# Optimization experiments

Measured on AMD Instinct MI355X. Metric: run time of the kernel, lower is better.

## Reference

```python
import jax, jax.numpy as jnp
import numpy as np

N, D = 2048, 1024
H, KV, HD = 16, 4, 64
REPEATS = H // KV
SCALE = HD ** -0.5


def setup_inputs() -> dict:
    key = jax.random.key(0)
    ks = jax.random.split(key, 6)
    x = jax.random.normal(ks[0], (N, D), dtype=jnp.float32)
    # rotary tables: cos/sin of interleaved-pair angles (llama-style view_as_complex)
    pos = jnp.arange(N, dtype=jnp.float32)[:, None]
    inv_freq = 1.0 / (10000.0 ** (jnp.arange(0, HD, 2, dtype=jnp.float32) / HD))
    ang = pos * inv_freq[None, :]  # (N, HD//2)
    freqs_cos = jnp.cos(ang)
    freqs_sin = jnp.sin(ang)
    s = 0.02
    Wq = jax.random.normal(ks[1], (D, H * HD), dtype=jnp.float32) * s
    Wk = jax.random.normal(ks[2], (D, KV * HD), dtype=jnp.float32) * s
    Wv = jax.random.normal(ks[3], (D, KV * HD), dtype=jnp.float32) * s
    Wo = jax.random.normal(ks[4], (H * HD, D), dtype=jnp.float32) * s
    return {"x": x, "freqs_cos": freqs_cos, "freqs_sin": freqs_sin,
            "Wq": Wq, "Wk": Wk, "Wv": Wv, "Wo": Wo}


def _rope(t, cos, sin):
    # t: (N, heads, HD); interleaved complex pairs (even=real, odd=imag)
    tr = t[..., 0::2]
    ti = t[..., 1::2]
    c = cos[:, None, :]
    s = sin[:, None, :]
    out_r = tr * c - ti * s
    out_i = tr * s + ti * c
    return jnp.stack([out_r, out_i], axis=-1).reshape(t.shape)


def reference(x, freqs_cos, freqs_sin, Wq, Wk, Wv, Wo):
    n = x.shape[0]
    xq = (x @ Wq).reshape(n, H, HD)
    xk = (x @ Wk).reshape(n, KV, HD)
    xv = (x @ Wv).reshape(n, KV, HD)
    xq = _rope(xq, freqs_cos, freqs_sin)
    xk = _rope(xk, freqs_cos, freqs_sin)
    # repeat_kv along head dim (GQA)
    k = jnp.repeat(xk, REPEATS, axis=1)  # (n, H, HD)
    v = jnp.repeat(xv, REPEATS, axis=1)
    # memory_efficient_attention with mask=None: full attention over token axis
    scores = jnp.einsum('nhd,mhd->hnm', xq, k) * SCALE
    attn = jax.nn.softmax(scores, axis=-1)
    out = jnp.einsum('hnm,mhd->nhd', attn, v)
    return out.reshape(n, H * HD) @ Wo
```

## Files before the change

### kernel.cpp

```cpp
#include <hip/hip_runtime.h>

#define N_TOK 2048
#define DMODEL 1024
#define NH 16
#define NKV 4
#define HDIM 64
#define SCALE_LOG2E 0.1803368801111204f

typedef __attribute__((ext_vector_type(8))) short short8;
typedef __attribute__((ext_vector_type(4))) float f32x4;
typedef __attribute__((ext_vector_type(16))) float f32x16;
typedef unsigned short u16;
typedef unsigned int u32;

__device__ __forceinline__ u16 f2bf(float x) {
    u32 u = __float_as_uint(x);
    u += 0x7FFF + ((u >> 16) & 1);
    return (u16)(u >> 16);
}
__device__ __forceinline__ u32 pack2(float a, float b) {
    return (u32)f2bf(a) | ((u32)f2bf(b) << 16);
}
__device__ __forceinline__ u32 pack2t(float a, float b) {
    return __builtin_amdgcn_perm(__float_as_uint(b), __float_as_uint(a), 0x07060302u);
}

__device__ __forceinline__ void gload16(const u16* g, u16* l) {
    __builtin_amdgcn_global_load_lds(
        (const __attribute__((address_space(1))) unsigned int*)g,
        (__attribute__((address_space(3))) unsigned int*)l, 16, 0, 0);
}

__global__ __launch_bounds__(256) void prep(
    const float* __restrict__ Wq, const float* __restrict__ Wk,
    const float* __restrict__ Wv, const float* __restrict__ Wo,
    const float* __restrict__ x,
    u16* __restrict__ Wqt, u16* __restrict__ Wkt, u16* __restrict__ Wvt,
    u16* __restrict__ Wot, u16* __restrict__ xb)
{
    const int z = blockIdx.z;
    const int t = threadIdx.x;
    if (z == 4) {
        size_t base = ((size_t)(blockIdx.y * 16 + blockIdx.x)) * 8192;
#pragma unroll
        for (int i = 0; i < 8; ++i) {
            float4 v = *(const float4*)(x + base + i * 1024 + t * 4);
            uint2 p; p.x = pack2(v.x, v.y); p.y = pack2(v.z, v.w);
            *(uint2*)(xb + base + i * 1024 + t * 4) = p;
        }
        return;
    }
    const float* W; u16* Wt; int NC;
    if      (z == 0) { W = Wq; Wt = Wqt; NC = 1024; }
    else if (z == 1) { W = Wk; Wt = Wkt; NC = 256; }
    else if (z == 2) { W = Wv; Wt = Wvt; NC = 256; }
    else             { W = Wo; Wt = Wot; NC = 1024; }
    const int n0 = blockIdx.x * 64;
    if (n0 >= NC) return;
    const int k0 = blockIdx.y * 64;
    __shared__ float T[64][68];
    const int row = t >> 2, cs = (t & 3) * 16;
#pragma unroll
    for (int i = 0; i < 4; ++i)
        *(float4*)&T[row][cs + i * 4] =
            *(const float4*)(W + (size_t)(k0 + row) * NC + n0 + cs + i * 4);
    __syncthreads();
    const int nl = t >> 2, ks = (t & 3) * 16;
    u32 pk[8];
#pragma unroll
    for (int i = 0; i < 8; ++i)
        pk[i] = pack2(T[ks + 2 * i][nl], T[ks + 2 * i + 1][nl]);
    u16* dst = Wt + (size_t)(n0 + nl) * DMODEL + k0 + ks;
    uint4 w0; w0.x = pk[0]; w0.y = pk[1]; w0.z = pk[2]; w0.w = pk[3];
    uint4 w1; w1.x = pk[4]; w1.y = pk[5]; w1.z = pk[6]; w1.w = pk[7];
    *(uint4*)(dst) = w0;
    *(uint4*)(dst + 8) = w1;
}

__global__ __launch_bounds__(256, 3) void gemm_qkv(
    const u16* __restrict__ A,
    const u16* __restrict__ B0, const u16* __restrict__ B1, const u16* __restrict__ B2,
    u16* __restrict__ D0, u16* __restrict__ D1, u16* __restrict__ FVout,
    const float* __restrict__ fc, const float* __restrict__ fs)
{
    __shared__ u16 As[2][64][64];
    __shared__ u16 Bs[2][64][64];
    const int t = threadIdx.x;
    const int m0 = blockIdx.x * 64;
    const int by = blockIdx.y;

    const u16* Bt; int nl0, ep;
    u16* dbf = nullptr; int dstride = 0; float epsc = 1.f;
    if (by < 16)      { Bt = B0; nl0 = by * 64;        dbf = D0; ep = 1; dstride = 1024;
                        epsc = SCALE_LOG2E; }
    else if (by < 20) { Bt = B1; nl0 = (by - 16) * 64; dbf = D1; ep = 1; dstride = 256; }
    else              { Bt = B2; nl0 = (by - 20) * 64; ep = 2; }

    const int w = t >> 6, lane = t & 63;
    const int quad = lane >> 4, l15 = lane & 15;
    const int wm = (w >> 1) * 32, wn = (w & 1) * 32;
    const int rx = l15 & 7;

    const int sro = w * 16 + (lane >> 3);
    const int sco = ((lane & 7) ^ (lane >> 3)) * 8;
    const u16* ApL = A + (size_t)(m0 + sro) * DMODEL + sco;
    const u16* BpL = Bt + (size_t)(nl0 + sro) * DMODEL + sco;

    f32x4 acc[2][2];
#pragma unroll
    for (int i = 0; i < 2; ++i)
#pragma unroll
        for (int j = 0; j < 2; ++j) acc[i][j] = {0.f, 0.f, 0.f, 0.f};

#pragma unroll
    for (int k = 0; k < 2; ++k) {
        gload16(ApL + k * 8 * DMODEL, &As[0][w * 16 + k * 8][0]);
        gload16(BpL + k * 8 * DMODEL, &Bs[0][w * 16 + k * 8][0]);
    }
    __syncthreads();

    for (int it = 0; it < 16; ++it) {
        const int cur = it & 1;
        if (it + 1 < 16) {
            const int kk = (it + 1) * 64;
#pragma unroll
            for (int k = 0; k < 2; ++k) {
                gload16(ApL + k * 8 * DMODEL + kk, &As[cur ^ 1][w * 16 + k * 8][0]);
                gload16(BpL + k * 8 * DMODEL + kk, &Bs[cur ^ 1][w * 16 + k * 8][0]);
            }
        }
#pragma unroll
        for (int c = 0; c < 2; ++c) {
            short8 af[2], bf[2];
#pragma unroll
            for (int i = 0; i < 2; ++i)
                af[i] = *(const short8*)&As[cur][wm + i * 16 + l15][((4 * c + quad) ^ rx) * 8];
#pragma unroll
            for (int j = 0; j < 2; ++j)
                bf[j] = *(const short8*)&Bs[cur][wn + j * 16 + l15][((4 * c + quad) ^ rx) * 8];
#pragma unroll
            for (int i = 0; i < 2; ++i)
#pragma unroll
                for (int j = 0; j < 2; ++j)
                    acc[i][j] = __builtin_amdgcn_mfma_f32_16x16x32_bf16(af[i], bf[j], acc[i][j], 0, 0, 0);
        }
        __syncthreads();
    }

#pragma unroll
    for (int i = 0; i < 2; ++i)
#pragma unroll
        for (int j = 0; j < 2; ++j) {
            const int cl = nl0 + wn + j * 16 + l15;
            if (ep == 1) {
#pragma unroll
                for (int r4 = 0; r4 < 4; ++r4) {
                    const int r = m0 + wm + i * 16 + quad * 4 + r4;
                    float own = acc[i][j][r4];
                    float other = __shfl_xor(own, 1, 64);
                    const int p = (cl & 63) >> 1;
                    const float c = fc[r * 32 + p] * epsc, s = fs[r * 32 + p] * epsc;
                    float outv = ((cl & 1) == 0) ? (own * c - other * s)
                                                 : (other * s + own * c);
                    dbf[(size_t)r * dstride + cl] = f2bf(outv);
                }
            } else {
                const int rb = m0 + wm + i * 16 + quad * 4;
                const int g = cl >> 6, d = cl & 63;
                const int d2 = d >> 5, dl = d & 31;
                const int keyblk = rb >> 7, kg = (rb >> 5) & 3;
                const int kst = (rb >> 4) & 1, hb = (rb >> 3) & 1, jv = rb & 7;
                size_t idx = ((((((size_t)(g * 16 + keyblk) * 4 + kg) * 2 + kst) * 2 + d2)
                               * 2 + hb) * 32 + dl) * 8 + jv;
                uint2 pk;
                pk.x = pack2(acc[i][j][0], acc[i][j][1]);
                pk.y = pack2(acc[i][j][2], acc[i][j][3]);
                *(uint2*)(FVout + idx) = pk;
            }
        }
}

__global__ __launch_bounds__(256, 2) void gemm_out(
    const u16* __restrict__ A, const u16* __restrict__ Bt, float* __restrict__ Dout)
{
    __shared__ u16 As[2][64][64];
    __shared__ u16 Bs[2][64][64];
    const int t = threadIdx.x;
    const int m0 = blockIdx.x * 64;
    const int nl0 = blockIdx.y * 64;

    const int w = t >> 6, lane = t & 63;
    const int quad = lane >> 4, l15 = lane & 15;
    const int wm = (w >> 1) * 32, wn = (w & 1) * 32;
    const int rx = l15 & 7;

    const int sro = w * 16 + (lane >> 3);
    const int sco = ((lane & 7) ^ (lane >> 3)) * 8;
    const u16* ApL = A + (size_t)(m0 + sro) * DMODEL + sco;
    const u16* BpL = Bt + (size_t)(nl0 + sro) * DMODEL + sco;

    f32x4 acc[2][2];
#pragma unroll
    for (int i = 0; i < 2; ++i)
#pragma unroll
        for (int j = 0; j < 2; ++j) acc[i][j] = {0.f, 0.f, 0.f, 0.f};

#pragma unroll
    for (int k = 0; k < 2; ++k) {
        gload16(ApL + k * 8 * DMODEL, &As[0][w * 16 + k * 8][0]);
        gload16(BpL + k * 8 * DMODEL, &Bs[0][w * 16 + k * 8][0]);
    }
    __syncthreads();

    for (int it = 0; it < 16; ++it) {
        const int cur = it & 1;
        if (it + 1 < 16) {
            const int kk = (it + 1) * 64;
#pragma unroll
            for (int k = 0; k < 2; ++k) {
                gload16(ApL + k * 8 * DMODEL + kk, &As[cur ^ 1][w * 16 + k * 8][0]);
                gload16(BpL + k * 8 * DMODEL + kk, &Bs[cur ^ 1][w * 16 + k * 8][0]);
            }
        }
#pragma unroll
        for (int c = 0; c < 2; ++c) {
            short8 af[2], bf[2];
#pragma unroll
            for (int i = 0; i < 2; ++i)
                af[i] = *(const short8*)&As[cur][wm + i * 16 + l15][((4 * c + quad) ^ rx) * 8];
#pragma unroll
            for (int j = 0; j < 2; ++j)
                bf[j] = *(const short8*)&Bs[cur][wn + j * 16 + l15][((4 * c + quad) ^ rx) * 8];
#pragma unroll
            for (int i = 0; i < 2; ++i)
#pragma unroll
                for (int j = 0; j < 2; ++j)
                    acc[i][j] = __builtin_amdgcn_mfma_f32_16x16x32_bf16(af[i], bf[j], acc[i][j], 0, 0, 0);
        }
        __syncthreads();
    }

#pragma unroll
    for (int i = 0; i < 2; ++i)
#pragma unroll
        for (int j = 0; j < 2; ++j) {
            const int cl = nl0 + wn + j * 16 + l15;
#pragma unroll
            for (int r4 = 0; r4 < 4; ++r4) {
                const int r = m0 + wm + i * 16 + quad * 4 + r4;
                Dout[(size_t)r * 1024 + cl] = acc[i][j][r4];
            }
        }
}

__global__ __launch_bounds__(256, 2) void attn(
    const u16* __restrict__ Qb, const u16* __restrict__ Kb,
    const u16* __restrict__ FV, u16* __restrict__ Ob)
{
    __shared__ u16 Ks[2][2][64][72];
    __shared__ u16 Ps[4][32][40];

    const int t = threadIdx.x;
    const int n0 = blockIdx.x * 64;
    const int h = blockIdx.y, kvh = h >> 2;
    const int w = t >> 6, lane = t & 63;
    const int hi = lane >> 5, l31 = lane & 31;
    const int qgrp = w & 1, khalf = w >> 1;
    const int srow = t >> 1, ssel = (t & 1) * 32;
    const int khalf_s = srow >> 6, klocal = srow & 63;

    const short8 ones = {(short)0x3F80, (short)0x3F80, (short)0x3F80, (short)0x3F80,
                         (short)0x3F80, (short)0x3F80, (short)0x3F80, (short)0x3F80};

    const u16* qp = Qb + (size_t)(n0 + qgrp * 32 + l31) * (NH * HDIM) + h * HDIM + hi * 8;
    short8 qf[4];
#pragma unroll
    for (int s = 0; s < 4; ++s) qf[s] = *(const short8*)(qp + s * 16);

    const u16* kbase = Kb + (size_t)(khalf_s * 1024 + klocal) * (NKV * HDIM) + kvh * HDIM + ssel;
    const u16* fvb = FV + ((size_t)kvh * 16 * 8192) + (size_t)lane * 8;

    f32x16 o[2], o_l;
#pragma unroll
    for (int d2 = 0; d2 < 2; ++d2)
#pragma unroll
        for (int r = 0; r < 16; ++r) o[d2][r] = 0.f;
#pragma unroll
    for (int r = 0; r < 16; ++r) o_l[r] = 0.f;

#pragma unroll
    for (int c = 0; c < 4; ++c)
        *(uint4*)&Ks[0][khalf_s][klocal][ssel + c * 8] = *(const uint4*)(kbase + c * 8);
    __syncthreads();

    for (int rd = 0; rd < 16; ++rd) {
        const int cur = rd & 1, nxt = cur ^ 1;
        const int rdn = (rd + 1) & 15;
        uint4 kr[4];
#pragma unroll
        for (int c = 0; c < 4; ++c)
            kr[c] = *(const uint4*)(kbase + (size_t)(rdn * 64) * (NKV * HDIM) + c * 8);

#pragma unroll
        for (int kg = 0; kg < 2; ++kg) {
            const int kg_global = khalf * 32 + rd * 2 + kg;
            const int keyblk = kg_global >> 2, kgi = kg_global & 3;
            short8 vf[2][2];
#pragma unroll
            for (int s = 0; s < 2; ++s)
#pragma unroll
                for (int d2 = 0; d2 < 2; ++d2)
                    vf[s][d2] = *(const short8*)(fvb +
                        ((((size_t)keyblk * 4 + kgi) * 2 + s) * 2 + d2) * 512);
            f32x16 sa;
#pragma unroll
            for (int r = 0; r < 16; ++r) sa[r] = 0.f;
#pragma unroll
            for (int s = 0; s < 4; ++s) {
                short8 kf = *(const short8*)&Ks[cur][khalf][kg * 32 + l31][s * 16 + hi * 8];
                sa = __builtin_amdgcn_mfma_f32_32x32x16_bf16(kf, qf[s], sa, 0, 0, 0);
            }
            float p[16];
#pragma unroll
            for (int r = 0; r < 16; ++r) p[r] = __builtin_amdgcn_exp2f(sa[r]);
#pragma unroll
            for (int blk = 0; blk < 4; ++blk) {
                uint2 pk;
                pk.x = pack2t(p[blk * 4 + 0], p[blk * 4 + 1]);
                pk.y = pack2t(p[blk * 4 + 2], p[blk * 4 + 3]);
                *(uint2*)&Ps[w][l31][blk * 8 + 4 * hi] = pk;
            }
            const short8 ap0 = *(const short8*)&Ps[w][l31][hi * 8];
            const short8 ap1 = *(const short8*)&Ps[w][l31][16 + hi * 8];
#pragma unroll
            for (int d2 = 0; d2 < 2; ++d2) {
                o[d2] = __builtin_amdgcn_mfma_f32_32x32x16_bf16(ap0, vf[0][d2], o[d2], 0, 0, 0);
                o[d2] = __builtin_amdgcn_mfma_f32_32x32x16_bf16(ap1, vf[1][d2], o[d2], 0, 0, 0);
            }
            o_l = __builtin_amdgcn_mfma_f32_32x32x16_bf16(ap0, ones, o_l, 0, 0, 0);
            o_l = __builtin_amdgcn_mfma_f32_32x32x16_bf16(ap1, ones, o_l, 0, 0, 0);
        }
#pragma unroll
        for (int c = 0; c < 4; ++c)
            *(uint4*)&Ks[nxt][khalf_s][klocal][ssel + c * 8] = kr[c];
        __syncthreads();
    }

    float* Xf = (float*)&Ks[0][0][0][0];
    if (khalf == 1) {
#pragma unroll
        for (int d2 = 0; d2 < 2; ++d2)
#pragma unroll
            for (int r = 0; r < 16; ++r) {
                const int q32 = (r & 3) + 8 * (r >> 2) + 4 * hi;
                Xf[qgrp * 2048 + q32 * 64 + d2 * 32 + l31] = o[d2][r];
            }
        if (l31 == 0) {
#pragma unroll
            for (int r = 0; r < 16; ++r) {
                const int q32 = (r & 3) + 8 * (r >> 2) + 4 * hi;
                Xf[4096 + qgrp * 32 + q32] = o_l[r];
            }
        }
    }
    __syncthreads();
    if (khalf == 0) {
        float linv[16];
#pragma unroll
        for (int r = 0; r < 16; ++r) {
            const int q32 = (r & 3) + 8 * (r >> 2) + 4 * hi;
            linv[r] = 1.f / (o_l[r] + Xf[4096 + qgrp * 32 + q32]);
        }
#pragma unroll
        for (int d2 = 0; d2 < 2; ++d2)
#pragma unroll
            for (int r = 0; r < 16; ++r) {
                const int q32 = (r & 3) + 8 * (r >> 2) + 4 * hi;
                const float val = o[d2][r] + Xf[qgrp * 2048 + q32 * 64 + d2 * 32 + l31];
                const int qrow = n0 + qgrp * 32 + q32;
                Ob[(size_t)qrow * (NH * HDIM) + h * HDIM + d2 * 32 + l31] = f2bf(val * linv[r]);
            }
    }
}

extern "C" void kernel_launch(void* const* d_in, const int* in_sizes, int n_in,
                              void* d_out, int out_size, void* d_ws, size_t ws_size,
                              hipStream_t stream) {
    const float* x  = (const float*)d_in[0];
    const float* fc = (const float*)d_in[1];
    const float* fs = (const float*)d_in[2];
    const float* Wq = (const float*)d_in[3];
    const float* Wk = (const float*)d_in[4];
    const float* Wv = (const float*)d_in[5];
    const float* Wo = (const float*)d_in[6];
    float* out = (float*)d_out;

    u16* ws  = (u16*)d_ws;
    u16* xb  = ws;
    u16* Wqt = xb  + (size_t)2048 * 1024;
    u16* Wkt = Wqt + (size_t)1024 * 1024;
    u16* Wvt = Wkt + (size_t)256 * 1024;
    u16* Wot = Wvt + (size_t)256 * 1024;
    u16* qb  = Wot + (size_t)1024 * 1024;
    u16* kb  = qb  + (size_t)2048 * 1024;
    u16* fv  = kb  + (size_t)2048 * 256;
    u16* aob = fv  + (size_t)256 * 2048;

    prep<<<dim3(16, 16, 5), dim3(256), 0, stream>>>(Wq, Wk, Wv, Wo, x,
                                                    Wqt, Wkt, Wvt, Wot, xb);
    gemm_qkv<<<dim3(32, 24), dim3(256), 0, stream>>>(xb, Wqt, Wkt, Wvt,
                                                     qb, kb, fv, fc, fs);
    attn<<<dim3(32, 16), dim3(256), 0, stream>>>(qb, kb, fv, aob);
    gemm_out<<<dim3(32, 16), dim3(256), 0, stream>>>(aob, Wot, out);
}
```

Measured before the change: 138.5 us.

## Replace LDS round-trip for P with permlane32 swaps; hoist V loads, add setprio

The attention inner loop used to write the bf16-packed probabilities to a per-wave LDS buffer and read them back as the MFMA A-operand. They are now rearranged in registers with permlane32_swap, which removes the Ps shared array and its LDS traffic. V fragment loads for both key groups are hoisted ahead of the compute so they are issued earlier. s_setprio is raised around the MFMA sections to favour matrix issue across waves. The costs are higher register pressure from the doubled V fragments and the risk of an incorrect lane mapping in the swap.

```diff
diff --git a/kernel.cpp b/kernel.cpp
--- a/kernel.cpp
+++ b/kernel.cpp
@@ -10,6 +10,8 @@
 typedef __attribute__((ext_vector_type(8))) short short8;
 typedef __attribute__((ext_vector_type(4))) float f32x4;
 typedef __attribute__((ext_vector_type(16))) float f32x16;
+typedef __attribute__((ext_vector_type(2))) int i32x2;
+typedef __attribute__((ext_vector_type(4))) unsigned int u32x4;
 typedef unsigned short u16;
 typedef unsigned int u32;
 
@@ -258,7 +260,6 @@
     const u16* __restrict__ FV, u16* __restrict__ Ob)
 {
     __shared__ u16 Ks[2][2][64][72];
-    __shared__ u16 Ps[4][32][40];
 
     const int t = threadIdx.x;
     const int n0 = blockIdx.x * 64;
@@ -301,44 +302,59 @@
         for (int c = 0; c < 4; ++c)
             kr[c] = *(const uint4*)(kbase + (size_t)(rdn * 64) * (NKV * HDIM) + c * 8);
 
+        short8 vf[2][2][2];
 #pragma unroll
         for (int kg = 0; kg < 2; ++kg) {
             const int kg_global = khalf * 32 + rd * 2 + kg;
             const int keyblk = kg_global >> 2, kgi = kg_global & 3;
-            short8 vf[2][2];
 #pragma unroll
             for (int s = 0; s < 2; ++s)
 #pragma unroll
                 for (int d2 = 0; d2 < 2; ++d2)
-                    vf[s][d2] = *(const short8*)(fvb +
+                    vf[kg][s][d2] = *(const short8*)(fvb +
                         ((((size_t)keyblk * 4 + kgi) * 2 + s) * 2 + d2) * 512);
+        }
+
+#pragma unroll
+        for (int kg = 0; kg < 2; ++kg) {
             f32x16 sa;
 #pragma unroll
             for (int r = 0; r < 16; ++r) sa[r] = 0.f;
+            __builtin_amdgcn_s_setprio(1);
 #pragma unroll
             for (int s = 0; s < 4; ++s) {
                 short8 kf = *(const short8*)&Ks[cur][khalf][kg * 32 + l31][s * 16 + hi * 8];
                 sa = __builtin_amdgcn_mfma_f32_32x32x16_bf16(kf, qf[s], sa, 0, 0, 0);
             }
+            __builtin_amdgcn_s_setprio(0);
             float p[16];
 #pragma unroll
             for (int r = 0; r < 16; ++r) p[r] = __builtin_amdgcn_exp2f(sa[r]);
-#pragma unroll
-            for (int blk = 0; blk < 4; ++blk) {
-                uint2 pk;
-                pk.x = pack2t(p[blk * 4 + 0], p[blk * 4 + 1]);
-                pk.y = pack2t(p[blk * 4 + 2], p[blk * 4 + 3]);
-                *(uint2*)&Ps[w][l31][blk * 8 + 4 * hi] = pk;
-            }
-            const short8 ap0 = *(const short8*)&Ps[w][l31][hi * 8];
-            const short8 ap1 = *(const short8*)&Ps[w][l31][16 + hi * 8];
+            const u32 A0 = pack2t(p[0],  p[1]);
+            const u32 B0 = pack2t(p[2],  p[3]);
+            const u32 C0 = pack2t(p[4],  p[5]);
+            const u32 D0 = pack2t(p[6],  p[7]);
+            const u32 E0 = pack2t(p[8],  p[9]);
+            const u32 F0 = pack2t(p[10], p[11]);
+            const u32 G0 = pack2t(p[12], p[13]);
+            const u32 H0 = pack2t(p[14], p[15]);
+            i32x2 X = __builtin_amdgcn_permlane32_swap((int)A0, (int)C0, false, false);
+            i32x2 Y = __builtin_amdgcn_permlane32_swap((int)B0, (int)D0, false, false);
+            i32x2 Z = __builtin_amdgcn_permlane32_swap((int)E0, (int)G0, false, false);
+            i32x2 U = __builtin_amdgcn_permlane32_swap((int)F0, (int)H0, false, false);
+            u32x4 t0 = {(u32)X.x, (u32)Y.x, (u32)X.y, (u32)Y.y};
+            u32x4 t1 = {(u32)Z.x, (u32)U.x, (u32)Z.y, (u32)U.y};
+            const short8 ap0 = __builtin_bit_cast(short8, t0);
+            const short8 ap1 = __builtin_bit_cast(short8, t1);
+            __builtin_amdgcn_s_setprio(1);
 #pragma unroll
             for (int d2 = 0; d2 < 2; ++d2) {
-                o[d2] = __builtin_amdgcn_mfma_f32_32x32x16_bf16(ap0, vf[0][d2], o[d2], 0, 0, 0);
-                o[d2] = __builtin_amdgcn_mfma_f32_32x32x16_bf16(ap1, vf[1][d2], o[d2], 0, 0, 0);
+                o[d2] = __builtin_amdgcn_mfma_f32_32x32x16_bf16(ap0, vf[kg][0][d2], o[d2], 0, 0, 0);
+                o[d2] = __builtin_amdgcn_mfma_f32_32x32x16_bf16(ap1, vf[kg][1][d2], o[d2], 0, 0, 0);
             }
             o_l = __builtin_amdgcn_mfma_f32_32x32x16_bf16(ap0, ones, o_l, 0, 0, 0);
             o_l = __builtin_amdgcn_mfma_f32_32x32x16_bf16(ap1, ones, o_l, 0, 0, 0);
+            __builtin_amdgcn_s_setprio(0);
         }
 #pragma unroll
         for (int c = 0; c < 4; ++c)
```

New measurement: 136.1 us. About the same (-1.7%).
